# Optimization experiments

Measured on AMD Instinct MI355X. Metric: run time of the kernel, lower is better.

The kernel has to match this reference:

```python
import jax, jax.numpy as jnp
import numpy as np

NUM_CP = 64
D_MODEL = 128
N = 1_000_000


def setup_inputs() -> dict:
    key = jax.random.key(0)
    k_t, k_cp = jax.random.split(key)
    t = jax.random.uniform(k_t, (N,), dtype=jnp.float32)  # in [0,1)
    control_points = jax.random.normal(k_cp, (NUM_CP, D_MODEL), dtype=jnp.float32) / np.sqrt(NUM_CP)
    return {"t": t, "control_points": control_points}


def reference(t, control_points):
    # Faithful to the torch loop:
    #   out = sum_{i=0}^{K-2} (1 - |t - i|) * cp[i]
    # Note: weights are NOT clamped to >=0 in the original, so we keep the
    # dense (possibly negative) triangular weights and express the sum as a
    # single [N, K-1] @ [K-1, D] matmul.
    t = jnp.clip(t, 0.0, 1.0)                         # [N]
    k = control_points.shape[0] - 1                   # K-1 terms in the loop
    idx = jnp.arange(k, dtype=t.dtype)                # [K-1]
    weights = 1.0 - jnp.abs(t[:, None] - idx[None, :])  # [N, K-1]
    return weights @ control_points[:-1]              # [N, D]
```

## Files before the change

### kernel.cpp

```cpp
#include <hip/hip_runtime.h>

#define NUM_CP 64
#define D_MODEL 128

typedef float f32x4 __attribute__((ext_vector_type(4)));

__global__ __launch_bounds__(256) void spline_fused(const float* __restrict__ t,
                                                    const float* __restrict__ cp,
                                                    float* __restrict__ out, int n) {
    __shared__ float sbc[2 * D_MODEL];

    const int tid = threadIdx.x;
    if (tid < D_MODEL) {
        float v0 = cp[tid];
        float B = v0, C = -v0;
        for (int i = 1; i < NUM_CP - 1; ++i) {
            float v = cp[i * D_MODEL + tid];
            B = fmaf(1.0f - (float)i, v, B);
            C += v;
        }
        sbc[tid] = B;
        sbc[D_MODEL + tid] = C;
    }
    __syncthreads();

    const int lane = tid & 63;
    const int c    = lane & 31;
    const int half = lane >> 5;

    const f32x4 b  = reinterpret_cast<const f32x4*>(sbc)[c];
    const f32x4 cv = reinterpret_cast<const f32x4*>(sbc + D_MODEL)[c];

    const int waveGlobal = blockIdx.x * 4 + (tid >> 6);
    const int nWaves     = gridDim.x * 4;
    const int rowStride  = nWaves * 8;
    f32x4* __restrict__ outq = reinterpret_cast<f32x4*>(out);

    int R0 = waveGlobal * 8;
    if (R0 >= n) return;

    bool full = (R0 + 7 < n);
    f32x4 ta, tb;
    if (full) {
        ta = *reinterpret_cast<const f32x4*>(t + R0);
        tb = *reinterpret_cast<const f32x4*>(t + R0 + 4);
    }

    for (; R0 < n; R0 += rowStride) {
        const int R0n = R0 + rowStride;
        const bool fulln = (R0n + 7 < n);
        f32x4 tan_, tbn;
        if (fulln) {
            tan_ = *reinterpret_cast<const f32x4*>(t + R0n);
            tbn  = *reinterpret_cast<const f32x4*>(t + R0n + 4);
        }

        if (full) {
            float tv[4];
            tv[0] = half ? ta.y : ta.x;
            tv[1] = half ? ta.w : ta.z;
            tv[2] = half ? tb.y : tb.x;
            tv[3] = half ? tb.w : tb.z;
#pragma unroll
            for (int k = 0; k < 4; ++k) tv[k] = fminf(fmaxf(tv[k], 0.0f), 1.0f);
#pragma unroll
            for (int k = 0; k < 4; ++k) {
                f32x4 o;
                o.x = fmaf(tv[k], cv.x, b.x);
                o.y = fmaf(tv[k], cv.y, b.y);
                o.z = fmaf(tv[k], cv.z, b.z);
                o.w = fmaf(tv[k], cv.w, b.w);
                __builtin_nontemporal_store(o, &outq[(R0 + 2 * k + half) * 32 + c]);
            }
        } else {
            for (int k = 0; k < 4; ++k) {
                const int r = R0 + 2 * k + half;
                if (r < n) {
                    float tv = fminf(fmaxf(t[r], 0.0f), 1.0f);
                    f32x4 o;
                    o.x = fmaf(tv, cv.x, b.x);
                    o.y = fmaf(tv, cv.y, b.y);
                    o.z = fmaf(tv, cv.z, b.z);
                    o.w = fmaf(tv, cv.w, b.w);
                    __builtin_nontemporal_store(o, &outq[r * 32 + c]);
                }
            }
        }
        ta = tan_;
        tb = tbn;
        full = fulln;
    }
}

extern "C" void kernel_launch(void* const* d_in, const int* in_sizes, int n_in,
                              void* d_out, int out_size, void* d_ws, size_t ws_size,
                              hipStream_t stream) {
    const float* t  = (const float*)d_in[0];
    const float* cp = (const float*)d_in[1];
    float* out = (float*)d_out;
    const int n = in_sizes[0];

    const int waveTasks  = (n + 7) / 8;
    const int wantBlocks = (waveTasks + 3) / 4;
    const int blocks = wantBlocks < 2048 ? wantBlocks : 2048;
    spline_fused<<<blocks, 256, 0, stream>>>(t, cp, out, n);
}
```

Measured before the change: 102.5 us.

## Assign each wave a contiguous 128-row chunk instead of grid-stride loop

Switches from a persistent grid-stride loop over a capped 2048-block grid to giving each wave a contiguous chunk of 128 rows, with the grid sized to cover all rows. Each wave now writes one contiguous 64 KB region of output, which may improve DRAM write locality. In exchange it launches about 1954 blocks, each of which redoes the 63-row control-point reduction into shared memory.

```diff
diff --git a/kernel.cpp b/kernel.cpp
--- a/kernel.cpp
+++ b/kernel.cpp
@@ -2,6 +2,7 @@
 
 #define NUM_CP 64
 #define D_MODEL 128
+#define RPW 128
 
 typedef float f32x4 __attribute__((ext_vector_type(4)));
 
@@ -32,27 +33,26 @@
     const f32x4 cv = reinterpret_cast<const f32x4*>(sbc + D_MODEL)[c];
 
     const int waveGlobal = blockIdx.x * 4 + (tid >> 6);
-    const int nWaves     = gridDim.x * 4;
-    const int rowStride  = nWaves * 8;
+    const int base = waveGlobal * RPW;
+    if (base >= n) return;
+    const int end = min(base + RPW, n);
     f32x4* __restrict__ outq = reinterpret_cast<f32x4*>(out);
 
-    int R0 = waveGlobal * 8;
-    if (R0 >= n) return;
-
-    bool full = (R0 + 7 < n);
+    int r0 = base;
+    bool full = (r0 + 7 < end);
     f32x4 ta, tb;
     if (full) {
-        ta = *reinterpret_cast<const f32x4*>(t + R0);
-        tb = *reinterpret_cast<const f32x4*>(t + R0 + 4);
+        ta = *reinterpret_cast<const f32x4*>(t + r0);
+        tb = *reinterpret_cast<const f32x4*>(t + r0 + 4);
     }
 
-    for (; R0 < n; R0 += rowStride) {
-        const int R0n = R0 + rowStride;
-        const bool fulln = (R0n + 7 < n);
+    for (; r0 < end; r0 += 8) {
+        const int r0n = r0 + 8;
+        const bool fulln = (r0n + 7 < end);
         f32x4 tan_, tbn;
         if (fulln) {
-            tan_ = *reinterpret_cast<const f32x4*>(t + R0n);
-            tbn  = *reinterpret_cast<const f32x4*>(t + R0n + 4);
+            tan_ = *reinterpret_cast<const f32x4*>(t + r0n);
+            tbn  = *reinterpret_cast<const f32x4*>(t + r0n + 4);
         }
 
         if (full) {
@@ -70,12 +70,12 @@
                 o.y = fmaf(tv[k], cv.y, b.y);
                 o.z = fmaf(tv[k], cv.z, b.z);
                 o.w = fmaf(tv[k], cv.w, b.w);
-                __builtin_nontemporal_store(o, &outq[(R0 + 2 * k + half) * 32 + c]);
+                __builtin_nontemporal_store(o, &outq[(r0 + 2 * k + half) * 32 + c]);
             }
         } else {
             for (int k = 0; k < 4; ++k) {
-                const int r = R0 + 2 * k + half;
-                if (r < n) {
+                const int r = r0 + 2 * k + half;
+                if (r < end) {
                     float tv = fminf(fmaxf(t[r], 0.0f), 1.0f);
                     f32x4 o;
                     o.x = fmaf(tv, cv.x, b.x);
@@ -100,8 +100,7 @@
     float* out = (float*)d_out;
     const int n = in_sizes[0];
 
-    const int waveTasks  = (n + 7) / 8;
-    const int wantBlocks = (waveTasks + 3) / 4;
-    const int blocks = wantBlocks < 2048 ? wantBlocks : 2048;
+    const int waves  = (n + RPW - 1) / RPW;
+    const int blocks = (waves + 3) / 4;
     spline_fused<<<blocks, 256, 0, stream>>>(t, cp, out, n);
 }
```

New measurement: 103.9 us. No clear change (+1.4%).
